# Optimization experiments

Hardware: AMD Instinct MI355X
Metric: run time of the kernel (lower is better)

Reference implementation:

```python
import jax, jax.numpy as jnp
import numpy as np

N = 4096          # num_nodes
M = 131072        # num_edges (chain + random)
H = 64            # hidden_size of DerivConstrainedPerceptron
DMIN = 0.5
DMAX = 2.0
LO = 1.0 / DMAX   # min slope of h_inv
HI = 1.0 / DMIN   # max slope of h_inv
MITR = 30         # fixed iteration count (early-exit at eps in the original; 30 iters converge far below eps here)
RIDGE = 1e-6      # numerical ridge on grounded Laplacian


def _h_inv(y, logits, w_raw, b):
    # Derivative-constrained perceptron: h_inv'(y) = LO + (HI-LO)*sum_k p_k*sigmoid(w_k*y+b_k) in (LO, HI).
    p = jax.nn.softmax(logits)                     # (H,)
    w = jax.nn.softplus(w_raw) + 1e-3              # (H,) positive slopes
    s = jax.nn.softplus(y[..., None] * w + b)      # (m, d, H)
    return LO * y + (HI - LO) * jnp.einsum('mdh,h->md', s, p / w)


def _chol_grounded(src, dst, w, n):
    # Dense weighted graph Laplacian L = A diag(w) A^T built by scatter-add, grounded at the last node.
    L = jnp.zeros((n, n), w.dtype)
    L = L.at[src, src].add(w).at[dst, dst].add(w)
    L = L.at[src, dst].add(-w).at[dst, src].add(-w)
    Lg = L[:-1, :-1] + RIDGE * jnp.eye(n - 1, dtype=w.dtype)
    return jnp.linalg.cholesky(Lg)


def _solve_grounded(c, rhs):
    # Solve L phi = rhs with the grounded node's potential fixed to 0 (valid for balanced rhs; only
    # potential differences phi[src]-phi[dst] are used, which equal A^T L^+ rhs).
    x = jax.scipy.linalg.cho_solve((c, True), rhs[:-1])
    return jnp.concatenate([x, jnp.zeros((1, rhs.shape[1]), rhs.dtype)], axis=0)


def _forward(u, edge_weights, logits, w_raw, b, src, dst):
    n = u.shape[0]
    w = edge_weights
    wcol = w[:, None]
    U = u[:, None]                                  # (n, 1) balanced injections
    At = lambda phi: phi[src] - phi[dst]            # incidence^T: node potentials -> edge diffs
    Amap = lambda z: jnp.zeros((n, z.shape[1]), z.dtype).at[src].add(z).at[dst].add(-z)  # incidence
    # get_f_cut: min-norm flow with A f_cut = U (unweighted Laplacian pseudo-solve)
    c0 = _chol_grounded(src, dst, jnp.ones_like(w), n)
    f_cut = At(_solve_grounded(c0, U))
    # weighted Laplacian factor for cycle_projection
    cw = _chol_grounded(src, dst, w, n)

    def cycle_projection(z):
        phi = _solve_grounded(cw, Amap(z))
        return z - wcol * At(phi)

    def step(f_cyc, _):
        y = (f_cyc + f_cut) / wcol
        z = f_cyc - DMIN * wcol * _h_inv(y, logits, w_raw, b)
        return cycle_projection(z), None

    f_cyc, _ = jax.lax.scan(step, jnp.zeros_like(f_cut), None, length=MITR)
    return (f_cyc + f_cut)[:, 0]                    # (m,) flows, squeezed as in IFNLayer.forward


def setup_inputs() -> dict:
    key = jax.random.key(0)
    k1, k2, k3, k4, k5, k6, k7 = jax.random.split(key, 7)
    # connected graph: chain spanning tree + random extra edges (no self-loops)
    src0 = jnp.arange(N - 1, dtype=jnp.int32)
    dst0 = src0 + 1
    extra = M - (N - 1)
    src1 = jax.random.randint(k1, (extra,), 0, N, dtype=jnp.int32)
    off = jax.random.randint(k2, (extra,), 1, N, dtype=jnp.int32)
    dst1 = (src1 + off) % N
    src = jnp.concatenate([src0, src1])
    dst = jnp.concatenate([dst0, dst1])
    edge_weights = 0.5 + jax.random.uniform(k3, (M,), jnp.float32)
    u = jax.random.normal(k4, (N,), jnp.float32)
    u = u - u.mean()                                # balanced nodal injections
    logits = 0.1 * jax.random.normal(k5, (H,), jnp.float32)
    w_raw = 0.1 * jax.random.normal(k6, (H,), jnp.float32)
    b = 0.1 * jax.random.normal(k7, (H,), jnp.float32)
    return {"u": u, "edge_weights": edge_weights, "logits": logits,
            "w_raw": w_raw, "b": b, "src": src, "dst": dst}


def reference(u, edge_weights, logits, w_raw, b, src, dst):
    return _forward(u, edge_weights, logits, w_raw, b, src, dst)
```

## Files before the change

### kernel.cpp

```cpp
#include <hip/hip_runtime.h>

#define NN 4096
#define MM 131072
#define HH 64
#define NB 128
#define NT 1024
#define NTH (NB*NT)
#define FB 512
#define FT 256
#define LPN 32
#define ELP 4
#define SLOTC 112
#define MITR 13
#define NPOL 1
#define CURS 16
#define TBL 4096
#define YMIN (-64.0f)
#define YMAX (64.0f)
#define INV_DY 32.0f

#define THETA 1.025f

static_assert(NTH == LPN*NN, "lanes-per-node mapping requires NTH == LPN*N");
static_assert(MM == FB*FT,   "one edge per thread in fill kernel");
static_assert(NN % NT == 0,  "LDS snapshot staging loop requires NN % NT == 0");
static_assert(HH == 32*2,    "htab build uses 32 lanes x 2 heads");
static_assert(ELP*LPN >= SLOTC, "register CSR must cover slot capacity");

constexpr size_t OFF_FLAGS = 0;
constexpr size_t OFF_CUR   = 1024;
constexpr size_t ZERO_BYTES = OFF_CUR + (size_t)NN*CURS*4;
constexpr size_t OFF_HTAB  = ZERO_BYTES;
constexpr size_t OFF_P0    = OFF_HTAB + 4104*4;
constexpr size_t OFF_P1    = OFF_P0   + NN*8;
constexpr size_t OFF_P2    = OFF_P1   + NN*8;
constexpr size_t OFF_SLOT  = OFF_P2   + NN*8;

__device__ __forceinline__ int cload_i(const int* p) {
    return __hip_atomic_load(p, __ATOMIC_RELAXED, __HIP_MEMORY_SCOPE_AGENT);
}
__device__ __forceinline__ unsigned long long cload64(const unsigned long long* p) {
    return __hip_atomic_load(p, __ATOMIC_RELAXED, __HIP_MEMORY_SCOPE_AGENT);
}
__device__ __forceinline__ void cstore64(unsigned long long* p, unsigned long long v) {
    __hip_atomic_store(p, v, __ATOMIC_RELAXED, __HIP_MEMORY_SCOPE_AGENT);
}
__device__ __forceinline__ unsigned long long pack2(float a, float b) {
    return ((unsigned long long)__float_as_uint(b) << 32) | __float_as_uint(a);
}

__device__ __forceinline__ float hinv_lds(float y, const float* __restrict__ hs) {
    float v;
    if (y <= YMIN) {
        v = hs[0];
    } else if (y >= YMAX) {
        v = hs[TBL] + (y - YMAX) * 1.5f;
    } else {
        float t = (y - YMIN) * INV_DY;
        int i = (int)t;
        if (i > TBL-1) i = TBL-1;
        float fr = t - (float)i;
        float h0 = hs[i];
        v = h0 + (hs[i+1] - h0) * fr;
    }
    return 0.5f*y + v;
}

__device__ __forceinline__ void fast_sync() {
    asm volatile("s_waitcnt lgkmcnt(0)" ::: "memory");
    __builtin_amdgcn_s_barrier();
    __builtin_amdgcn_sched_barrier(0);
}

__device__ __forceinline__ void grid_bar_full(int* flags, int& phase) {
    __syncthreads();
    phase += 1;
    if (threadIdx.x == 0) {
        __hip_atomic_store(&flags[blockIdx.x], phase,
                           __ATOMIC_RELAXED, __HIP_MEMORY_SCOPE_AGENT);
    }
    if (threadIdx.x < 64) {
        int lane = threadIdx.x;
        for (;;) {
            int a = cload_i(&flags[lane]);
            int b = cload_i(&flags[lane+64]);
            if (min(a, b) >= phase) break;
            __builtin_amdgcn_s_sleep(1);
        }
    }
    __syncthreads();
}

__global__ __launch_bounds__(FT) void fill_kernel(
    const float* __restrict__ ew,
    const int* __restrict__ src, const int* __restrict__ dst,
    const float* __restrict__ logits, const float* __restrict__ w_raw,
    const float* __restrict__ bb,
    char* __restrict__ ws)
{
    int*   cur   = (int*)  (ws + OFF_CUR);
    float* htab  = (float*)(ws + OFF_HTAB);
    unsigned long long* slots = (unsigned long long*)(ws + OFF_SLOT);

    const int g = blockIdx.x*FT + threadIdx.x;

    int a0 = src[g], d0 = dst[g];
    float w0 = ew[g];
    int p0 = atomicAdd(&cur[a0*CURS], 1);
    int p1 = atomicAdd(&cur[d0*CURS], 1);
    unsigned long long wb0 = ((unsigned long long)__float_as_uint(w0)) << 32;
    slots[(size_t)a0*SLOTC + p0] = wb0 | (unsigned int)(d0 | (g << 12));
    slots[(size_t)d0*SLOTC + p1] =
        wb0 | ((unsigned int)(a0 | (g << 12)) | 0x80000000u);

    {
        const int e0 = g >> 5;
        const int hl = (g & 31) << 1;
        float ex0 = expf(logits[hl+0]);
        float ex1 = expf(logits[hl+1]);
        float dsum = ex0 + ex1;
        dsum += __shfl_xor(dsum, 1);  dsum += __shfl_xor(dsum, 2);
        dsum += __shfl_xor(dsum, 4);  dsum += __shfl_xor(dsum, 8);
        dsum += __shfl_xor(dsum, 16);
        float wh0 = log1pf(expf(w_raw[hl+0])) + 0.001f;
        float wh1 = log1pf(expf(w_raw[hl+1])) + 0.001f;
        float c0 = (ex0/dsum)/wh0, c1 = (ex1/dsum)/wh1;
        float b0 = bb[hl+0], b1 = bb[hl+1];

        auto entry_acc = [&](float y) {
            float x0 = y*wh0 + b0, x1 = y*wh1 + b1;
            float sp0 = (x0 > 20.f) ? x0 : log1pf(expf(x0));
            float sp1 = (x1 > 20.f) ? x1 : log1pf(expf(x1));
            return c0*sp0 + c1*sp1;
        };

        float acc = entry_acc(YMIN + (float)e0 * (1.0f/INV_DY));
        acc += __shfl_xor(acc, 1);  acc += __shfl_xor(acc, 2);
        acc += __shfl_xor(acc, 4);  acc += __shfl_xor(acc, 8);
        acc += __shfl_xor(acc, 16);
        if ((g & 31) == 0) htab[e0] = 1.5f * acc;
        if (e0 == 0) {
            float acc2 = entry_acc(YMAX);
            acc2 += __shfl_xor(acc2, 1);  acc2 += __shfl_xor(acc2, 2);
            acc2 += __shfl_xor(acc2, 4);  acc2 += __shfl_xor(acc2, 8);
            acc2 += __shfl_xor(acc2, 16);
            if ((g & 31) == 0) htab[TBL] = 1.5f * acc2;
        }
    }
}

__global__ __launch_bounds__(NT) void main_kernel(
    const float* __restrict__ u,
    char* __restrict__ ws, float* __restrict__ out)
{
    int*   flags = (int*)  (ws + OFF_FLAGS);
    const int*   cur  = (const int*)  (ws + OFF_CUR);
    const float* htab = (const float*)(ws + OFF_HTAB);
    unsigned long long* P[3] = {
        (unsigned long long*)(ws + OFF_P0),
        (unsigned long long*)(ws + OFF_P1),
        (unsigned long long*)(ws + OFF_P2) };
    const unsigned long long* slots = (const unsigned long long*)(ws + OFF_SLOT);

    const int tid = threadIdx.x;
    const int g   = blockIdx.x*NT + tid;
    const int n   = g / LPN;
    const int s   = g % LPN;
    int phase = 0;

    __shared__ float hs[TBL+1];
    __shared__ unsigned long long ps[NN];

    for (int t = tid; t <= TBL; t += NT) hs[t] = htab[t];

    float u_reg = (s == 0) ? u[n] : 0.f;
    const int   deg = cur[n*CURS];
    const float dg0 = (float)deg;

    int   cidx[ELP];
    float cw[ELP];
    float cwinv[ELP];
    float cmask[ELP];
    float csgn[ELP];
    int   ceid[ELP];
    float zz_s[ELP];
    #pragma unroll
    for (int j = 0; j < ELP; ++j) {
        int sl  = s + j*LPN;
        bool ok = sl < deg;
        unsigned long long v = ok ? slots[(size_t)n*SLOTC + sl] : 0ull;
        unsigned int meta = (unsigned int)v;
        float w  = ok ? __uint_as_float((unsigned int)(v >> 32)) : 0.f;
        int   c  = (int)(meta & 0xFFFu);
        cidx[j]  = c;
        cw[j]    = w;
        ceid[j]  = (int)((meta >> 12) & 0x1FFFFu);
        csgn[j]  = ok ? (((int)meta < 0) ? -1.f : 1.f) : 0.f;
        cmask[j] = ok ? 1.f : 0.f;
        cwinv[j] = ok ? 1.0f / w : 0.f;
        zz_s[j]  = 0.f;
    }
    float wdn = 0.f;
    #pragma unroll
    for (int j = 0; j < ELP; ++j) wdn += cw[j];
    wdn += __shfl_xor(wdn, 1);  wdn += __shfl_xor(wdn, 2);
    wdn += __shfl_xor(wdn, 4);  wdn += __shfl_xor(wdn, 8);
    wdn += __shfl_xor(wdn, 16);

    float phiw_reg = 0.f;
    float phi0_reg = 0.f;
    const float inv_tw = 1.0f / (THETA * wdn);
    const float inv_t0 = 1.0f / (THETA * dg0);

    __syncthreads();

    int cb = 0;
    unsigned long long pf[NN/NT];

    for (int it = 0; it < MITR + NPOL; ++it) {
        const bool zact = (it < MITR);

        if (it > 0) {
            #pragma unroll
            for (int k = 0; k < NN/NT; ++k) ps[tid + k*NT] = pf[k];
        }
        float phiw_self = __shfl(phiw_reg, 0, LPN);
        float phi0_self = __shfl(phi0_reg, 0, LPN);
        if (it > 0) fast_sync();

        float acc0 = 0.f;
        float accr = 0.f;
        #pragma unroll
        for (int j = 0; j < ELP; ++j) {
            unsigned long long v = (it > 0) ? ps[cidx[j]] : 0ull;
            float pw = __uint_as_float((unsigned int)v);
            float p0 = __uint_as_float((unsigned int)(v >> 32));
            acc0 += cmask[j] * p0;
            float dphi = csgn[j] * (phiw_self - pw);
            float z;
            if (zact) {
                float fcut = csgn[j] * (phi0_self - p0);
                float fc = (it == 0) ? 0.f : (zz_s[j] - cw[j]*dphi);
                float y = (fc + fcut) * cwinv[j];
                float h = hinv_lds(y, hs);
                z = fc - 0.5f*cw[j]*h;
                zz_s[j] = z;
            } else {
                z = zz_s[j];
            }
            accr += csgn[j] * (z - cw[j]*dphi);
        }
        acc0 += __shfl_xor(acc0, 1);  acc0 += __shfl_xor(acc0, 2);
        acc0 += __shfl_xor(acc0, 4);  acc0 += __shfl_xor(acc0, 8);
        acc0 += __shfl_xor(acc0, 16);
        accr += __shfl_xor(accr, 1);  accr += __shfl_xor(accr, 2);
        accr += __shfl_xor(accr, 4);  accr += __shfl_xor(accr, 8);
        accr += __shfl_xor(accr, 16);
        if (s == 0) {
            float r0 = u_reg - (dg0*phi0_reg - acc0);
            phi0_reg += r0 * inv_t0;
            phiw_reg += accr * inv_tw;
            cstore64(&P[(cb+1)%3][n], pack2(phiw_reg, phi0_reg));
        }
        if (it < MITR + NPOL - 1) {
            __syncthreads();
            phase += 1;
            if (tid == 0) {
                __hip_atomic_store(&flags[blockIdx.x], phase,
                                   __ATOMIC_RELAXED, __HIP_MEMORY_SCOPE_AGENT);
            }
            __builtin_amdgcn_sched_barrier(0);
            #pragma unroll
            for (int k = 0; k < NN/NT; ++k) {
                pf[k] = cload64(&P[(cb+1)%3][tid + k*NT]);
            }
            if (tid < 64) {
                int need = phase - ((it == MITR - 1) ? 1 : 2);
                for (;;) {
                    int a = cload_i(&flags[tid]);
                    int b = cload_i(&flags[tid+64]);
                    if (min(a, b) >= need) break;
                    __builtin_amdgcn_s_sleep(1);
                }
            }
        } else {
            grid_bar_full(flags, phase);
        }
        cb = (cb + 1) % 3;
    }

    {
        #pragma unroll
        for (int k = 0; k < NN/NT; ++k) {
            int t = tid + k*NT;
            ps[t] = cload64(&P[cb][t]);
        }
        float phiw_self = __shfl(phiw_reg, 0, LPN);
        float phi0_self = __shfl(phi0_reg, 0, LPN);
        __syncthreads();
        #pragma unroll
        for (int j = 0; j < ELP; ++j) {
            if (csgn[j] > 0.5f) {
                unsigned long long v = ps[cidx[j]];
                float pw = __uint_as_float((unsigned int)v);
                float p0 = __uint_as_float((unsigned int)(v >> 32));
                float dphi = phiw_self - pw;
                float fcut = phi0_self - p0;
                float fc   = zz_s[j] - cw[j]*dphi;
                out[ceid[j]] = fc + fcut;
            }
        }
    }
}

extern "C" void kernel_launch(void* const* d_in, const int* in_sizes, int n_in,
                              void* d_out, int out_size, void* d_ws, size_t ws_size,
                              hipStream_t stream) {
    const float* u      = (const float*)d_in[0];
    const float* ew     = (const float*)d_in[1];
    const float* logits = (const float*)d_in[2];
    const float* w_raw  = (const float*)d_in[3];
    const float* b      = (const float*)d_in[4];
    const int*   src    = (const int*)d_in[5];
    const int*   dst    = (const int*)d_in[6];
    float* out = (float*)d_out;
    char* ws = (char*)d_ws;

    hipMemsetAsync(ws, 0, ZERO_BYTES, stream);
    fill_kernel<<<FB, FT, 0, stream>>>(ew, src, dst, logits, w_raw, b, ws);
    main_kernel<<<NB, NT, 0, stream>>>(u, ws, out);
}
```

Baseline: 143.9 us.

## Gather neighbor potentials directly from global memory instead of LDS snapshot

Each iteration previously copied the whole 4096-entry potential vector into LDS with coalesced loads, then ran a block barrier before the per-edge neighbor lookups. Now each lane loads only its own up to four neighbor entries straight from the global triple buffer. This removes the per-iteration LDS staging and block sync, at the cost of scattered 8-byte global/L2 loads. Iteration 0 now uses a full grid barrier so the first gather sees complete data. The slot CSR loads are also issued before the degree load to overlap their latency.

```diff
diff --git a/kernel.cpp b/kernel.cpp
--- a/kernel.cpp
+++ b/kernel.cpp
@@ -23,7 +23,6 @@
 
 static_assert(NTH == LPN*NN, "lanes-per-node mapping requires NTH == LPN*N");
 static_assert(MM == FB*FT,   "one edge per thread in fill kernel");
-static_assert(NN % NT == 0,  "LDS snapshot staging loop requires NN % NT == 0");
 static_assert(HH == 32*2,    "htab build uses 32 lanes x 2 heads");
 static_assert(ELP*LPN >= SLOTC, "register CSR must cover slot capacity");
 
@@ -66,12 +65,6 @@
     return 0.5f*y + v;
 }
 
-__device__ __forceinline__ void fast_sync() {
-    asm volatile("s_waitcnt lgkmcnt(0)" ::: "memory");
-    __builtin_amdgcn_s_barrier();
-    __builtin_amdgcn_sched_barrier(0);
-}
-
 __device__ __forceinline__ void grid_bar_full(int* flags, int& phase) {
     __syncthreads();
     phase += 1;
@@ -169,11 +162,18 @@
     int phase = 0;
 
     __shared__ float hs[TBL+1];
-    __shared__ unsigned long long ps[NN];
 
     for (int t = tid; t <= TBL; t += NT) hs[t] = htab[t];
 
     float u_reg = (s == 0) ? u[n] : 0.f;
+
+    unsigned long long vraw[ELP];
+    #pragma unroll
+    for (int j = 0; j < ELP; ++j) {
+        int sl = s + j*LPN;
+        int slc = (sl < SLOTC) ? sl : (SLOTC-1);
+        vraw[j] = slots[(size_t)n*SLOTC + slc];
+    }
     const int   deg = cur[n*CURS];
     const float dg0 = (float)deg;
 
@@ -188,7 +188,7 @@
     for (int j = 0; j < ELP; ++j) {
         int sl  = s + j*LPN;
         bool ok = sl < deg;
-        unsigned long long v = ok ? slots[(size_t)n*SLOTC + sl] : 0ull;
+        unsigned long long v = ok ? vraw[j] : 0ull;
         unsigned int meta = (unsigned int)v;
         float w  = ok ? __uint_as_float((unsigned int)(v >> 32)) : 0.f;
         int   c  = (int)(meta & 0xFFFu);
@@ -215,24 +215,19 @@
     __syncthreads();
 
     int cb = 0;
-    unsigned long long pf[NN/NT];
+    unsigned long long pf[ELP];
 
     for (int it = 0; it < MITR + NPOL; ++it) {
         const bool zact = (it < MITR);
 
-        if (it > 0) {
-            #pragma unroll
-            for (int k = 0; k < NN/NT; ++k) ps[tid + k*NT] = pf[k];
-        }
         float phiw_self = __shfl(phiw_reg, 0, LPN);
         float phi0_self = __shfl(phi0_reg, 0, LPN);
-        if (it > 0) fast_sync();
 
         float acc0 = 0.f;
         float accr = 0.f;
         #pragma unroll
         for (int j = 0; j < ELP; ++j) {
-            unsigned long long v = (it > 0) ? ps[cidx[j]] : 0ull;
+            unsigned long long v = (it > 0) ? pf[j] : 0ull;
             float pw = __uint_as_float((unsigned int)v);
             float p0 = __uint_as_float((unsigned int)(v >> 32));
             acc0 += cmask[j] * p0;
@@ -262,7 +257,13 @@
             phiw_reg += accr * inv_tw;
             cstore64(&P[(cb+1)%3][n], pack2(phiw_reg, phi0_reg));
         }
-        if (it < MITR + NPOL - 1) {
+
+        if (it == 0) {
+            grid_bar_full(flags, phase);
+            #pragma unroll
+            for (int j = 0; j < ELP; ++j)
+                pf[j] = cload64(&P[(cb+1)%3][cidx[j]]);
+        } else if (it < MITR + NPOL - 1) {
             __syncthreads();
             phase += 1;
             if (tid == 0) {
@@ -271,9 +272,8 @@
             }
             __builtin_amdgcn_sched_barrier(0);
             #pragma unroll
-            for (int k = 0; k < NN/NT; ++k) {
-                pf[k] = cload64(&P[(cb+1)%3][tid + k*NT]);
-            }
+            for (int j = 0; j < ELP; ++j)
+                pf[j] = cload64(&P[(cb+1)%3][cidx[j]]);
             if (tid < 64) {
                 int need = phase - ((it == MITR - 1) ? 1 : 2);
                 for (;;) {
@@ -290,18 +290,12 @@
     }
 
     {
-        #pragma unroll
-        for (int k = 0; k < NN/NT; ++k) {
-            int t = tid + k*NT;
-            ps[t] = cload64(&P[cb][t]);
-        }
         float phiw_self = __shfl(phiw_reg, 0, LPN);
         float phi0_self = __shfl(phi0_reg, 0, LPN);
-        __syncthreads();
         #pragma unroll
         for (int j = 0; j < ELP; ++j) {
             if (csgn[j] > 0.5f) {
-                unsigned long long v = ps[cidx[j]];
+                unsigned long long v = cload64(&P[cb][cidx[j]]);
                 float pw = __uint_as_float((unsigned int)v);
                 float p0 = __uint_as_float((unsigned int)(v >> 32));
                 float dphi = phiw_self - pw;
```

Measured after the change: 145.0 us. About the same (+0.7%).
